# Kernel tuning notes

Measured on AMD Instinct MI355X. Metric: run time of the kernel, lower is better.

## Reference

```python
import jax, jax.numpy as jnp
import numpy as np

BASE_R = 0.1      # base_radius (compared against squared distances)
K = 20            # PositionEncoder k
H = 0.1           # dilated_ball_query bandwidth
EPS_BN = 1e-5


def _gelu(x):
    return jax.nn.gelu(x, approximate=False)  # torch nn.GELU default (erf)


def _bn(x, g, b):
    # eval-mode BatchNorm (running_mean=0, running_var=1), channel axis = 1
    shape = (1, -1) + (1,) * (x.ndim - 2)
    scale = g / np.float32(np.sqrt(1.0 + EPS_BN))
    return x * scale.reshape(shape) + b.reshape(shape)


def _conv1x1(x, w):
    # pointwise conv (no bias): w [out_c, in_c], x [B, in_c, ...]
    return jnp.einsum('oc,bc...->bo...', w, x)


def _l1norm(x, axis):
    # F.normalize(p=1): divide by L1 norm clamped to 1e-12
    return x / jnp.maximum(jnp.sum(jnp.abs(x), axis=axis, keepdims=True), 1e-12)


def _forward(xyz, w_q, g_q, b_q, w_k, g_k, b_k, w_v, g_v, b_v,
             w_pe, b_pe, g_pe, bb_pe, w_m1, g_m1, b_m1, w_m2, g_m2, b_m2,
             w_out, g_out, b_out):
    B, _, N = xyz.shape
    # ---- pairwise squared distances [B,N,N] ----
    sq = jnp.sum(xyz * xyz, axis=1)
    dist = -2.0 * jnp.einsum('bcn,bcm->bnm', xyz, xyz) + sq[:, :, None] + sq[:, None, :]
    # ---- dilated ball query (sigma=1) ----
    gauss = jnp.exp(-dist / (2.0 * H * H))
    kd = jnp.sum(gauss, axis=-1, keepdims=True)                 # [B,N,1]
    kd_score = kd / (jnp.max(kd, axis=1, keepdims=True) + 1e-9)
    radius = BASE_R + BASE_R * kd_score                         # max_radius = 2*base
    keep = dist < radius                                        # [B,N,N]
    # ---- masked attention (emb_cent == emb_x == cat(xyz, xyz)) ----
    emb = jnp.concatenate([xyz, xyz], axis=1)                   # [B,6,N]
    q = _bn(_conv1x1(emb, w_q), g_q, b_q)                       # [B,1,N]
    k_ = _bn(_conv1x1(emb, w_k), g_k, b_k)                      # [B,1,N]
    scores = jnp.einsum('bhn,bhm->bnm', q, k_)                  # [B,N,N]
    scores = jnp.where(keep, scores, -1e9)
    adj = jax.nn.softmax(scores, axis=-1)
    adj = _l1norm(_l1norm(adj, 1), -1)                          # doubly L1-normalized
    # ---- graph smoothing + value conv ----
    smoothed = jnp.einsum('bcn,bnm->bcm', xyz, adj)
    variation = smoothed - xyz
    v = _bn(_conv1x1(jnp.concatenate([variation, xyz], axis=1), w_v), g_v, b_v)  # [B,64,N]
    # ---- position encoder: ball-query top-k neighbor gather ----
    ar = jnp.arange(N, dtype=jnp.int32)[None, None, :]
    idx = jnp.where(dist > radius, N, ar)                       # mark out-of-ball with N
    idx = jnp.sort(idx, axis=-1)[:, :, :K]                      # k nearest-index in-ball
    idx = jnp.where(idx == N, idx[:, :, :1], idx)               # pad with first neighbor
    grouped = jax.vmap(lambda f, i: f[:, i])(xyz, idx)          # [B,3,N,K]
    pts = jnp.broadcast_to(xyz[:, :, :, None], grouped.shape)
    pf = jnp.concatenate([pts, grouped, grouped - pts], axis=1)  # [B,9,N,K]
    pf = _conv1x1(pf, w_pe) + b_pe[None, :, None, None]          # conv2d 1x1 with bias
    pf = _gelu(_bn(pf, g_pe, bb_pe))
    pf = jnp.max(pf, axis=-1)                                    # [B,out/8,N]
    pf = _gelu(_bn(_conv1x1(pf, w_m1), g_m1, b_m1))              # [B,out/4,N]
    pos = _bn(_conv1x1(pf, w_m2), g_m2, b_m2)                    # [B,out,N]
    out = _gelu(v + pos)
    return _bn(_conv1x1(out, w_out), g_out, b_out)               # [B,32,N]


def setup_inputs() -> dict:
    key = jax.random.key(0)
    ks = iter(jax.random.split(key, 40))
    B, N, OC = 4, 4096, 64

    def w(shape):
        return jax.random.normal(next(ks), shape, jnp.float32) / np.float32(np.sqrt(shape[-1]))

    def gb(c):
        g = 1.0 + 0.1 * jax.random.normal(next(ks), (c,), jnp.float32)
        b = 0.1 * jax.random.normal(next(ks), (c,), jnp.float32)
        return g, b

    xyz = jax.random.uniform(next(ks), (B, 3, N), jnp.float32)
    g_q, b_q = gb(1)
    g_k, b_k = gb(1)
    g_v, b_v = gb(OC)
    g_pe, bb_pe = gb(OC // 8)
    g_m1, b_m1 = gb(OC // 4)
    g_m2, b_m2 = gb(OC)
    g_out, b_out = gb(32)
    return {
        'xyz': xyz,
        'w_q': w((1, 6)), 'g_q': g_q, 'b_q': b_q,
        'w_k': w((1, 6)), 'g_k': g_k, 'b_k': b_k,
        'w_v': w((OC, 6)), 'g_v': g_v, 'b_v': b_v,
        'w_pe': w((OC // 8, 9)), 'b_pe': 0.1 * jax.random.normal(next(ks), (OC // 8,), jnp.float32),
        'g_pe': g_pe, 'bb_pe': bb_pe,
        'w_m1': w((OC // 4, OC // 8)), 'g_m1': g_m1, 'b_m1': b_m1,
        'w_m2': w((OC, OC // 4)), 'g_m2': g_m2, 'b_m2': b_m2,
        'w_out': w((32, OC)), 'g_out': g_out, 'b_out': b_out,
    }


def reference(xyz, w_q, g_q, b_q, w_k, g_k, b_k, w_v, g_v, b_v,
              w_pe, b_pe, g_pe, bb_pe, w_m1, g_m1, b_m1, w_m2, g_m2, b_m2,
              w_out, g_out, b_out):
    return _forward(xyz, w_q, g_q, b_q, w_k, g_k, b_k, w_v, g_v, b_v,
                    w_pe, b_pe, g_pe, bb_pe, w_m1, g_m1, b_m1, w_m2, g_m2, b_m2,
                    w_out, g_out, b_out)
```

## Files before the change

### kernel.cpp

```cpp
#include <hip/hip_runtime.h>
#include <math.h>

#define BB 4
#define NN 4096
#define KNBR 20
#define BN (BB * NN)
#define NSLICE 8
#define SLEN (NN / NSLICE)
#define JPW (SLEN / 16)

#define LOG2E 1.44269504088896340736f

typedef __attribute__((ext_vector_type(2))) float v2f;

__device__ __forceinline__ v2f fma2(v2f a, v2f b, v2f c) {
    return __builtin_elementwise_fma(a, b, c);
}
__device__ __forceinline__ v2f splat2(float s) { v2f r; r.x = s; r.y = s; return r; }

__device__ __forceinline__ float gelu_f(float x) {
    return 0.5f * x * (1.0f + erff(x * 0.70710678118654752440f));
}

__device__ __forceinline__ float4 mkrec(const float* __restrict__ xb, int n) {
    float x = xb[n], y = xb[NN + n], z = xb[2 * NN + n];
    float sq = fmaf(x, x, fmaf(y, y, z * z));
    return make_float4(x, y, z, sq);
}

__global__ void k0_prep(const float* __restrict__ xyz, float4* __restrict__ pts4) {
    int t = blockIdx.x * blockDim.x + threadIdx.x;
    if (t >= BN) return;
    int b = t / NN, n = t % NN;
    pts4[t] = mkrec(xyz + (size_t)b * 3 * NN, n);
}


__global__ __launch_bounds__(1024, 8)
void p1_kd(const float4* __restrict__ pts4, float* __restrict__ part) {
    __shared__ float s_red[16][256];
    int tid = threadIdx.x;
    int wave = __builtin_amdgcn_readfirstlane(tid >> 6);
    int lane = tid & 63;
    int g = blockIdx.x >> 3, slice = blockIdx.x & 7;
    int b = g >> 4;
    const float4* rb = pts4 + (size_t)b * NN + slice * SLEN + wave * JPW;
    v2f frx[2], fry[2], frz[2], frw[2];
    v2f acc[2] = {splat2(0.f), splat2(0.f)};
    #pragma unroll
    for (int h = 0; h < 2; ++h) {
        float4 r0 = pts4[g * 256 + (2 * h) * 64 + lane];
        float4 r1 = pts4[g * 256 + (2 * h + 1) * 64 + lane];
        frx[h].x = r0.x; frx[h].y = r1.x;
        fry[h].x = r0.y; fry[h].y = r1.y;
        frz[h].x = r0.z; frz[h].y = r1.z;
        frw[h].x = r0.w; frw[h].y = r1.w;
    }
    const v2f m2 = splat2(-2.0f);
    const float C1 = -50.0f * LOG2E;
    #pragma unroll 4
    for (int j = 0; j < JPW; ++j) {
        float4 fc = rb[j];
        #pragma unroll
        for (int h = 0; h < 2; ++h) {
            v2f dot = frx[h] * fc.x + fry[h] * fc.y + frz[h] * fc.z;
            v2f d = fma2(m2, dot, frw[h]) + fc.w;
            v2f arg = d * C1;
            acc[h].x += __builtin_amdgcn_exp2f(arg.x);
            acc[h].y += __builtin_amdgcn_exp2f(arg.y);
        }
    }
    #pragma unroll
    for (int h = 0; h < 2; ++h) {
        s_red[wave][(2 * h) * 64 + lane] = acc[h].x;
        s_red[wave][(2 * h + 1) * 64 + lane] = acc[h].y;
    }
    __syncthreads();
    if (tid < 256) {
        float s = 0.f;
        #pragma unroll
        for (int w = 0; w < 16; ++w) s += s_red[w][tid];
        part[slice * BN + g * 256 + tid] = s;
    }
}

__global__ void k2_radius(const float* __restrict__ part, const float4* __restrict__ pts4,
                          const float* __restrict__ w_q, const float* __restrict__ g_q, const float* __restrict__ b_q,
                          const float* __restrict__ w_k, const float* __restrict__ g_k, const float* __restrict__ b_k,
                          float4* __restrict__ recB) {
    int b = blockIdx.x;
    int t = threadIdx.x;
    const float invs = rsqrtf(1.0f + 1e-5f);
    float kdv[4];
    float mx = -1e30f;
    #pragma unroll
    for (int j = 0; j < 4; ++j) {
        int n = b * NN + j * 1024 + t;
        float s = 0.f;
        #pragma unroll
        for (int c = 0; c < NSLICE; ++c) s += part[c * BN + n];
        kdv[j] = s;
        mx = fmaxf(mx, s);
    }
    __shared__ float red[1024];
    red[t] = mx;
    __syncthreads();
    for (int s = 512; s > 0; s >>= 1) {
        if (t < s) red[t] = fmaxf(red[t], red[t + s]);
        __syncthreads();
    }
    float kmax = red[0];
    #pragma unroll
    for (int j = 0; j < 4; ++j) {
        int n = b * NN + j * 1024 + t;
        float rad = 0.1f + 0.1f * (kdv[j] / (kmax + 1e-9f));
        float4 r = pts4[n];
        float qr = r.x * (w_q[0] + w_q[3]) + r.y * (w_q[1] + w_q[4]) + r.z * (w_q[2] + w_q[5]);
        float kr = r.x * (w_k[0] + w_k[3]) + r.y * (w_k[1] + w_k[4]) + r.z * (w_k[2] + w_k[5]);
        float q = qr * (g_q[0] * invs) + b_q[0];
        float k = kr * (g_k[0] * invs) + b_k[0];
        recB[2 * n] = r;
        recB[2 * n + 1] = make_float4(k, q, rad, 0.f);
    }
}

__global__ __launch_bounds__(1024, 8)
void p3_Zk7(const float4* __restrict__ recB, float* __restrict__ part,
            int* __restrict__ idxg) {
    __shared__ float s_red[16][256];
    int tid = threadIdx.x;
    int wave = __builtin_amdgcn_readfirstlane(tid >> 6);
    int lane = tid & 63;
    int g = blockIdx.x >> 3, slice = blockIdx.x & 7;
    int b = g >> 4;
    const float4* rb = recB + ((size_t)b * NN + slice * SLEN + wave * JPW) * 2;
    v2f frx[2], fry[2], frz[2], frw[2], ql2[2], rad[2];
    v2f acc[2] = {splat2(0.f), splat2(0.f)};
    #pragma unroll
    for (int h = 0; h < 2; ++h) {
        int r0i = g * 256 + (2 * h) * 64 + lane;
        int r1i = g * 256 + (2 * h + 1) * 64 + lane;
        float4 r0 = recB[2 * r0i], a0 = recB[2 * r0i + 1];
        float4 r1 = recB[2 * r1i], a1 = recB[2 * r1i + 1];
        frx[h].x = r0.x; frx[h].y = r1.x;
        fry[h].x = r0.y; fry[h].y = r1.y;
        frz[h].x = r0.z; frz[h].y = r1.z;
        frw[h].x = r0.w; frw[h].y = r1.w;
        ql2[h].x = a0.y * LOG2E; ql2[h].y = a1.y * LOG2E;
        rad[h].x = a0.z; rad[h].y = a1.z;
    }
    const v2f m2 = splat2(-2.0f);
    #pragma unroll 4
    for (int j = 0; j < JPW; ++j) {
        float4 fc = rb[2 * j];
        float4 an = rb[2 * j + 1];
        #pragma unroll
        for (int h = 0; h < 2; ++h) {
            v2f dot = frx[h] * fc.x + fry[h] * fc.y + frz[h] * fc.z;
            v2f d = fma2(m2, dot, frw[h]) + fc.w;
            v2f arg = ql2[h] * an.x;
            float e0 = __builtin_amdgcn_exp2f(arg.x);
            float e1 = __builtin_amdgcn_exp2f(arg.y);
            acc[h].x += (d.x < rad[h].x) ? e0 : 0.f;
            acc[h].y += (d.y < rad[h].y) ? e1 : 0.f;
        }
    }
    #pragma unroll
    for (int h = 0; h < 2; ++h) {
        s_red[wave][(2 * h) * 64 + lane] = acc[h].x;
        s_red[wave][(2 * h + 1) * 64 + lane] = acc[h].y;
    }
    __syncthreads();
    if (tid < 256) {
        float s = 0.f;
        #pragma unroll
        for (int w = 0; w < 16; ++w) s += s_red[w][tid];
        part[slice * BN + g * 256 + tid] = s;
    }
    int gw = blockIdx.x * 16 + wave;
    for (int rr = 0; rr < 2; ++rr) {
        int row7 = gw * 2 + rr;
        int b7 = row7 / NN;
        const float4* p7 = recB + (size_t)b7 * NN * 2;
        float4 f7 = recB[2 * row7];
        float rad7 = recB[2 * row7 + 1].z;
        int total = 0, firstm = 0;
        bool have = false;
        unsigned long long lmask = (1ULL << lane) - 1ULL;
        for (int i = 0; i < NN / 64 && total < KNBR; ++i) {
            int m = i * 64 + lane;
            float4 fc = p7[2 * m];
            float dot = f7.x * fc.x + f7.y * fc.y + f7.z * fc.z;
            float d = fmaf(-2.0f, dot, f7.w) + fc.w;
            bool inb = !(d > rad7);
            unsigned long long mask = __ballot(inb);
            if (!have && mask != 0ULL) {
                int src7 = __ffsll(mask) - 1;
                firstm = __shfl(m, src7);
                have = true;
            }
            int pos = total + (int)__popcll(mask & lmask);
            if (inb && pos < KNBR) idxg[(size_t)row7 * KNBR + pos] = m;
            total += (int)__popcll(mask);
        }
        if (total < KNBR && lane >= total && lane < KNBR)
            idxg[(size_t)row7 * KNBR + lane] = firstm;
    }
}

__global__ __launch_bounds__(1024, 8)
void p4_colsum(const float4* __restrict__ recB, const float* __restrict__ part3,
               float* __restrict__ part) {
    __shared__ float s_red[16][256];
    __shared__ float s_lnZ[SLEN];
    int tid = threadIdx.x;
    int wave = __builtin_amdgcn_readfirstlane(tid >> 6);
    int lane = tid & 63;
    int g = blockIdx.x >> 3, slice = blockIdx.x & 7;
    int b = g >> 4;
    if (tid < SLEN) {
        int gn = b * NN + slice * SLEN + tid;
        float s = 0.f;
        #pragma unroll
        for (int c = 0; c < NSLICE; ++c) s += part3[c * BN + gn];
        s_lnZ[tid] = __log2f(s);
    }
    const float4* rb = recB + ((size_t)b * NN + slice * SLEN + wave * JPW) * 2;
    v2f fcx[2], fcy[2], fcz[2], fcw[2], km2[2];
    v2f acc[2] = {splat2(0.f), splat2(0.f)};
    #pragma unroll
    for (int h = 0; h < 2; ++h) {
        int c0 = g * 256 + (2 * h) * 64 + lane;
        int c1 = g * 256 + (2 * h + 1) * 64 + lane;
        float4 r0 = recB[2 * c0], a0 = recB[2 * c0 + 1];
        float4 r1 = recB[2 * c1], a1 = recB[2 * c1 + 1];
        fcx[h].x = r0.x; fcx[h].y = r1.x;
        fcy[h].x = r0.y; fcy[h].y = r1.y;
        fcz[h].x = r0.z; fcz[h].y = r1.z;
        fcw[h].x = r0.w; fcw[h].y = r1.w;
        km2[h].x = a0.x * LOG2E; km2[h].y = a1.x * LOG2E;
    }
    __syncthreads();
    const v2f m2 = splat2(-2.0f);
    #pragma unroll 4
    for (int j = 0; j < JPW; ++j) {
        float4 fc = rb[2 * j];
        float4 an = rb[2 * j + 1];
        float lnZ2 = s_lnZ[wave * JPW + j];
        #pragma unroll
        for (int h = 0; h < 2; ++h) {
            v2f dot = fcx[h] * fc.x + fcy[h] * fc.y + fcz[h] * fc.z;
            v2f d = fma2(m2, dot, splat2(fc.w)) + fcw[h];
            v2f arg = fma2(splat2(an.y), km2[h], splat2(-lnZ2));
            float e0 = __builtin_amdgcn_exp2f(arg.x);
            float e1 = __builtin_amdgcn_exp2f(arg.y);
            acc[h].x += (d.x < an.z) ? e0 : 0.f;
            acc[h].y += (d.y < an.z) ? e1 : 0.f;
        }
    }
    #pragma unroll
    for (int h = 0; h < 2; ++h) {
        s_red[wave][(2 * h) * 64 + lane] = acc[h].x;
        s_red[wave][(2 * h + 1) * 64 + lane] = acc[h].y;
    }
    __syncthreads();
    if (tid < 256) {
        float s = 0.f;
        #pragma unroll
        for (int w = 0; w < 16; ++w) s += s_red[w][tid];
        part[slice * BN + g * 256 + tid] = s;
    }
}

__global__ __launch_bounds__(1024, 8)
void p5_rs(const float4* __restrict__ recB, const float* __restrict__ part5,
           float* __restrict__ part) {
    __shared__ float s_red[16][256];
    __shared__ float s_lnc[SLEN];
    int tid = threadIdx.x;
    int wave = __builtin_amdgcn_readfirstlane(tid >> 6);
    int lane = tid & 63;
    int g = blockIdx.x >> 3, slice = blockIdx.x & 7;
    int b = g >> 4;
    if (tid < SLEN) {
        int gm = b * NN + slice * SLEN + tid;
        float s = 0.f;
        #pragma unroll
        for (int c = 0; c < NSLICE; ++c) s += part5[c * BN + gm];
        s_lnc[tid] = __log2f(fmaxf(s, 1e-12f));
    }
    const float4* rb = recB + ((size_t)b * NN + slice * SLEN + wave * JPW) * 2;
    v2f frx[2], fry[2], frz[2], frw[2], ql2[2], rad[2];
    v2f acc[2] = {splat2(0.f), splat2(0.f)};
    #pragma unroll
    for (int h = 0; h < 2; ++h) {
        int r0i = g * 256 + (2 * h) * 64 + lane;
        int r1i = g * 256 + (2 * h + 1) * 64 + lane;
        float4 r0 = recB[2 * r0i], a0 = recB[2 * r0i + 1];
        float4 r1 = recB[2 * r1i], a1 = recB[2 * r1i + 1];
        frx[h].x = r0.x; frx[h].y = r1.x;
        fry[h].x = r0.y; fry[h].y = r1.y;
        frz[h].x = r0.z; frz[h].y = r1.z;
        frw[h].x = r0.w; frw[h].y = r1.w;
        ql2[h].x = a0.y * LOG2E; ql2[h].y = a1.y * LOG2E;
        rad[h].x = a0.z; rad[h].y = a1.z;
    }
    __syncthreads();
    const v2f m2 = splat2(-2.0f);
    #pragma unroll 4
    for (int j = 0; j < JPW; ++j) {
        float4 fc = rb[2 * j];
        float km = rb[2 * j + 1].x;
        float lnc2 = s_lnc[wave * JPW + j];
        #pragma unroll
        for (int h = 0; h < 2; ++h) {
            v2f dot = frx[h] * fc.x + fry[h] * fc.y + frz[h] * fc.z;
            v2f d = fma2(m2, dot, frw[h]) + fc.w;
            v2f arg = fma2(splat2(km), ql2[h], splat2(-lnc2));
            float e0 = __builtin_amdgcn_exp2f(arg.x);
            float e1 = __builtin_amdgcn_exp2f(arg.y);
            acc[h].x += (d.x < rad[h].x) ? e0 : 0.f;
            acc[h].y += (d.y < rad[h].y) ? e1 : 0.f;
        }
    }
    #pragma unroll
    for (int h = 0; h < 2; ++h) {
        s_red[wave][(2 * h) * 64 + lane] = acc[h].x;
        s_red[wave][(2 * h + 1) * 64 + lane] = acc[h].y;
    }
    __syncthreads();
    if (tid < 256) {
        float s = 0.f;
        #pragma unroll
        for (int w = 0; w < 16; ++w) s += s_red[w][tid];
        part[slice * BN + g * 256 + tid] = s;
    }
}

__global__ __launch_bounds__(1024, 8)
void p6_smooth(const float4* __restrict__ recB, const float* __restrict__ part3,
               const float* __restrict__ part7,
               float* __restrict__ partx, float* __restrict__ party,
               float* __restrict__ partz) {
    __shared__ float s_rx[16][256];
    __shared__ float s_ry[16][256];
    __shared__ float s_rz[16][256];
    __shared__ float s_w[SLEN];
    int tid = threadIdx.x;
    int wave = __builtin_amdgcn_readfirstlane(tid >> 6);
    int lane = tid & 63;
    int g = blockIdx.x >> 3, slice = blockIdx.x & 7;
    int b = g >> 4;
    if (tid < SLEN) {
        int gn = b * NN + slice * SLEN + tid;
        float sZ = 0.f, s7 = 0.f;
        #pragma unroll
        for (int c = 0; c < NSLICE; ++c) {
            sZ += part3[c * BN + gn];
            s7 += part7[c * BN + gn];
        }
        float rs = fmaxf(s7 / sZ, 1e-12f);
        s_w[tid] = __log2f(sZ) + __log2f(rs);
    }
    const float4* rb = recB + ((size_t)b * NN + slice * SLEN + wave * JPW) * 2;
    v2f fcx[2], fcy[2], fcz[2], fcw[2], km2[2];
    v2f ax[2] = {splat2(0.f), splat2(0.f)};
    v2f ay[2] = {splat2(0.f), splat2(0.f)};
    v2f az[2] = {splat2(0.f), splat2(0.f)};
    #pragma unroll
    for (int h = 0; h < 2; ++h) {
        int c0 = g * 256 + (2 * h) * 64 + lane;
        int c1 = g * 256 + (2 * h + 1) * 64 + lane;
        float4 r0 = recB[2 * c0], a0 = recB[2 * c0 + 1];
        float4 r1 = recB[2 * c1], a1 = recB[2 * c1 + 1];
        fcx[h].x = r0.x; fcx[h].y = r1.x;
        fcy[h].x = r0.y; fcy[h].y = r1.y;
        fcz[h].x = r0.z; fcz[h].y = r1.z;
        fcw[h].x = r0.w; fcw[h].y = r1.w;
        km2[h].x = a0.x * LOG2E; km2[h].y = a1.x * LOG2E;
    }
    __syncthreads();
    const v2f m2 = splat2(-2.0f);
    #pragma unroll 2
    for (int j = 0; j < JPW; ++j) {
        float4 fc = rb[2 * j];
        float4 an = rb[2 * j + 1];
        float w2j = s_w[wave * JPW + j];
        #pragma unroll
        for (int h = 0; h < 2; ++h) {
            v2f dot = fcx[h] * fc.x + fcy[h] * fc.y + fcz[h] * fc.z;
            v2f d = fma2(m2, dot, splat2(fc.w)) + fcw[h];
            v2f arg = fma2(splat2(an.y), km2[h], splat2(-w2j));
            float e0 = __builtin_amdgcn_exp2f(arg.x);
            float e1 = __builtin_amdgcn_exp2f(arg.y);
            v2f w;
            w.x = (d.x < an.z) ? e0 : 0.f;
            w.y = (d.y < an.z) ? e1 : 0.f;
            ax[h] = fma2(splat2(fc.x), w, ax[h]);
            ay[h] = fma2(splat2(fc.y), w, ay[h]);
            az[h] = fma2(splat2(fc.z), w, az[h]);
        }
    }
    #pragma unroll
    for (int h = 0; h < 2; ++h) {
        s_rx[wave][(2 * h) * 64 + lane] = ax[h].x;
        s_rx[wave][(2 * h + 1) * 64 + lane] = ax[h].y;
        s_ry[wave][(2 * h) * 64 + lane] = ay[h].x;
        s_ry[wave][(2 * h + 1) * 64 + lane] = ay[h].y;
        s_rz[wave][(2 * h) * 64 + lane] = az[h].x;
        s_rz[wave][(2 * h + 1) * 64 + lane] = az[h].y;
    }
    __syncthreads();
    if (tid < 256) {
        float sx = 0.f, sy = 0.f, sz = 0.f;
        #pragma unroll
        for (int w = 0; w < 16; ++w) {
            sx += s_rx[w][tid];
            sy += s_ry[w][tid];
            sz += s_rz[w][tid];
        }
        int o = slice * BN + g * 256 + tid;
        partx[o] = sx;
        party[o] = sy;
        partz[o] = sz;
    }
}

__global__ void k8_final(const float* __restrict__ xyz,
                         const float* __restrict__ partx, const float* __restrict__ party,
                         const float* __restrict__ partz, const float* __restrict__ part5,
                         const int* __restrict__ idxg,
                         const float* __restrict__ w_v, const float* __restrict__ g_v, const float* __restrict__ b_v,
                         const float* __restrict__ w_pe, const float* __restrict__ b_pe,
                         const float* __restrict__ g_pe, const float* __restrict__ bb_pe,
                         const float* __restrict__ w_m1, const float* __restrict__ g_m1, const float* __restrict__ b_m1,
                         const float* __restrict__ w_m2, const float* __restrict__ g_m2, const float* __restrict__ b_m2,
                         const float* __restrict__ w_out, const float* __restrict__ g_out, const float* __restrict__ b_out,
                         float* __restrict__ out) {
    __shared__ float s_pf8[32][9];
    __shared__ float s_pf16[32][17];
    __shared__ float s_g64[32][65];
    int tid = threadIdx.x;
    int ptL = tid >> 3, o = tid & 7;
    int p = blockIdx.x * 32 + ptL;
    int b = p / NN, n = p % NN;
    const float* xb = xyz + (size_t)b * 3 * NN;
    float x = xb[n], y = xb[NN + n], z = xb[2 * NN + n];
    const float invs = rsqrtf(1.0f + 1e-5f);

    float w0 = w_pe[o * 9 + 0], w1 = w_pe[o * 9 + 1], w2 = w_pe[o * 9 + 2];
    float w3 = w_pe[o * 9 + 3], w4 = w_pe[o * 9 + 4], w5 = w_pe[o * 9 + 5];
    float w6 = w_pe[o * 9 + 6], w7 = w_pe[o * 9 + 7], w8 = w_pe[o * 9 + 8];
    float bp = b_pe[o], gp = g_pe[o] * invs, bbp = bb_pe[o];
    float mx = -1e30f;
    for (int kk = 0; kk < KNBR; ++kk) {
        int j = idxg[(size_t)p * KNBR + kk];
        float gx = xb[j], gy = xb[NN + j], gz = xb[2 * NN + j];
        float dx = gx - x, dy = gy - y, dz = gz - z;
        float s = w0 * x + w1 * y + w2 * z + w3 * gx + w4 * gy + w5 * gz
                + w6 * dx + w7 * dy + w8 * dz + bp;
        s = gelu_f(s * gp + bbp);
        mx = fmaxf(mx, s);
    }
    s_pf8[ptL][o] = mx;
    __syncthreads();

    #pragma unroll
    for (int rr = 0; rr < 2; ++rr) {
        int r = o + rr * 8;
        const float* w = w_m1 + r * 8;
        float s = 0.f;
        #pragma unroll
        for (int c = 0; c < 8; ++c) s += w[c] * s_pf8[ptL][c];
        s_pf16[ptL][r] = gelu_f(s * (g_m1[r] * invs) + b_m1[r]);
    }
    __syncthreads();

    float cs = 0.f, sx = 0.f, sy = 0.f, sz = 0.f;
    #pragma unroll
    for (int c = 0; c < NSLICE; ++c) {
        cs += part5[c * BN + p];
        sx += partx[c * BN + p];
        sy += party[c * BN + p];
        sz += partz[c * BN + p];
    }
    float inv = 1.0f / fmaxf(cs, 1e-12f);
    float vx = sx * inv - x, vy = sy * inv - y, vz = sz * inv - z;
    #pragma unroll
    for (int i = 0; i < 8; ++i) {
        int ch = o * 8 + i;
        const float* wm = w_m2 + ch * 16;
        float pos = 0.f;
        #pragma unroll
        for (int c = 0; c < 16; ++c) pos += wm[c] * s_pf16[ptL][c];
        pos = pos * (g_m2[ch] * invs) + b_m2[ch];
        const float* wv = w_v + ch * 6;
        float vv = wv[0] * vx + wv[1] * vy + wv[2] * vz + wv[3] * x + wv[4] * y + wv[5] * z;
        vv = vv * (g_v[ch] * invs) + b_v[ch];
        s_g64[ptL][ch] = gelu_f(vv + pos);
    }
    __syncthreads();

    #pragma unroll
    for (int i = 0; i < 4; ++i) {
        int ch = o * 4 + i;
        const float* w = w_out + ch * 64;
        float s = 0.f;
        #pragma unroll
        for (int c = 0; c < 64; ++c) s += w[c] * s_g64[ptL][c];
        out[((size_t)b * 32 + ch) * NN + n] = s * (g_out[ch] * invs) + b_out[ch];
    }
}

extern "C" void kernel_launch(void* const* d_in, const int* in_sizes, int n_in,
                              void* d_out, int out_size, void* d_ws, size_t ws_size,
                              hipStream_t stream) {
    const float* xyz  = (const float*)d_in[0];
    const float* w_q  = (const float*)d_in[1];
    const float* g_q  = (const float*)d_in[2];
    const float* b_q  = (const float*)d_in[3];
    const float* w_k  = (const float*)d_in[4];
    const float* g_k  = (const float*)d_in[5];
    const float* b_k  = (const float*)d_in[6];
    const float* w_v  = (const float*)d_in[7];
    const float* g_v  = (const float*)d_in[8];
    const float* b_v  = (const float*)d_in[9];
    const float* w_pe = (const float*)d_in[10];
    const float* b_pe = (const float*)d_in[11];
    const float* g_pe = (const float*)d_in[12];
    const float* bb_pe= (const float*)d_in[13];
    const float* w_m1 = (const float*)d_in[14];
    const float* g_m1 = (const float*)d_in[15];
    const float* b_m1 = (const float*)d_in[16];
    const float* w_m2 = (const float*)d_in[17];
    const float* g_m2 = (const float*)d_in[18];
    const float* b_m2 = (const float*)d_in[19];
    const float* w_out= (const float*)d_in[20];
    const float* g_out= (const float*)d_in[21];
    const float* b_out= (const float*)d_in[22];

    float* ws = (float*)d_ws;
    float4* pts4   = (float4*)ws;
    float4* recB   = (float4*)(ws + (size_t)4  * BN);
    int*    idxg   = (int*)   (ws + (size_t)12 * BN);
    float*  part1  = ws + (size_t)32 * BN;
    float*  part3  = ws + (size_t)40 * BN;
    float*  part5  = ws + (size_t)48 * BN;
    float*  part7  = ws + (size_t)56 * BN;
    float*  partx  = ws + (size_t)64 * BN;
    float*  party  = ws + (size_t)72 * BN;
    float*  partz  = ws + (size_t)80 * BN;

    const int PB = (BN / 256) * NSLICE;

    k0_prep<<<BN / 256, 256, 0, stream>>>(xyz, pts4);
    p1_kd<<<PB, 1024, 0, stream>>>(pts4, part1);
    k2_radius<<<BB, 1024, 0, stream>>>(part1, pts4, w_q, g_q, b_q, w_k, g_k, b_k, recB);
    p3_Zk7<<<PB, 1024, 0, stream>>>(recB, part3, idxg);
    p4_colsum<<<PB, 1024, 0, stream>>>(recB, part3, part5);
    p5_rs<<<PB, 1024, 0, stream>>>(recB, part5, part7);
    p6_smooth<<<PB, 1024, 0, stream>>>(recB, part3, part7, partx, party, partz);
    k8_final<<<BN / 32, 256, 0, stream>>>(xyz, partx, party, partz, part5, idxg,
                                          w_v, g_v, b_v,
                                          w_pe, b_pe, g_pe, bb_pe,
                                          w_m1, g_m1, b_m1,
                                          w_m2, g_m2, b_m2,
                                          w_out, g_out, b_out,
                                          (float*)d_out);
}
```

Baseline: 234.9 us.

## Retile pairwise passes to 512-thread blocks with 8 rows per lane and 32 slices

```diff
diff --git a/kernel.cpp b/kernel.cpp
--- a/kernel.cpp
+++ b/kernel.cpp
@@ -5,9 +5,9 @@
 #define NN 4096
 #define KNBR 20
 #define BN (BB * NN)
-#define NSLICE 8
+#define NSLICE 32
 #define SLEN (NN / NSLICE)
-#define JPW (SLEN / 16)
+#define JPW (SLEN / 8)
 
 #define LOG2E 1.44269504088896340736f
 
@@ -36,21 +36,21 @@
 }
 
 
-__global__ __launch_bounds__(1024, 8)
+__global__ __launch_bounds__(512, 6)
 void p1_kd(const float4* __restrict__ pts4, float* __restrict__ part) {
-    __shared__ float s_red[16][256];
+    __shared__ float s_red[8][512];
     int tid = threadIdx.x;
     int wave = __builtin_amdgcn_readfirstlane(tid >> 6);
     int lane = tid & 63;
-    int g = blockIdx.x >> 3, slice = blockIdx.x & 7;
-    int b = g >> 4;
+    int g = blockIdx.x >> 5, slice = blockIdx.x & 31;
+    int b = g >> 3;
     const float4* rb = pts4 + (size_t)b * NN + slice * SLEN + wave * JPW;
-    v2f frx[2], fry[2], frz[2], frw[2];
-    v2f acc[2] = {splat2(0.f), splat2(0.f)};
-    #pragma unroll
-    for (int h = 0; h < 2; ++h) {
-        float4 r0 = pts4[g * 256 + (2 * h) * 64 + lane];
-        float4 r1 = pts4[g * 256 + (2 * h + 1) * 64 + lane];
+    v2f frx[4], fry[4], frz[4], frw[4];
+    v2f acc[4] = {splat2(0.f), splat2(0.f), splat2(0.f), splat2(0.f)};
+    #pragma unroll
+    for (int h = 0; h < 4; ++h) {
+        float4 r0 = pts4[g * 512 + (2 * h) * 64 + lane];
+        float4 r1 = pts4[g * 512 + (2 * h + 1) * 64 + lane];
         frx[h].x = r0.x; frx[h].y = r1.x;
         fry[h].x = r0.y; fry[h].y = r1.y;
         frz[h].x = r0.z; frz[h].y = r1.z;
@@ -58,11 +58,11 @@
     }
     const v2f m2 = splat2(-2.0f);
     const float C1 = -50.0f * LOG2E;
-    #pragma unroll 4
+    #pragma unroll 2
     for (int j = 0; j < JPW; ++j) {
         float4 fc = rb[j];
         #pragma unroll
-        for (int h = 0; h < 2; ++h) {
+        for (int h = 0; h < 4; ++h) {
             v2f dot = frx[h] * fc.x + fry[h] * fc.y + frz[h] * fc.z;
             v2f d = fma2(m2, dot, frw[h]) + fc.w;
             v2f arg = d * C1;
@@ -71,16 +71,16 @@
         }
     }
     #pragma unroll
-    for (int h = 0; h < 2; ++h) {
+    for (int h = 0; h < 4; ++h) {
         s_red[wave][(2 * h) * 64 + lane] = acc[h].x;
         s_red[wave][(2 * h + 1) * 64 + lane] = acc[h].y;
     }
     __syncthreads();
-    if (tid < 256) {
-        float s = 0.f;
-        #pragma unroll
-        for (int w = 0; w < 16; ++w) s += s_red[w][tid];
-        part[slice * BN + g * 256 + tid] = s;
+    {
+        float s = 0.f;
+        #pragma unroll
+        for (int w = 0; w < 8; ++w) s += s_red[w][tid];
+        part[slice * BN + g * 512 + tid] = s;
     }
 }
 
@@ -124,22 +124,22 @@
     }
 }
 
-__global__ __launch_bounds__(1024, 8)
+__global__ __launch_bounds__(512, 6)
 void p3_Zk7(const float4* __restrict__ recB, float* __restrict__ part,
             int* __restrict__ idxg) {
-    __shared__ float s_red[16][256];
+    __shared__ float s_red[8][512];
     int tid = threadIdx.x;
     int wave = __builtin_amdgcn_readfirstlane(tid >> 6);
     int lane = tid & 63;
-    int g = blockIdx.x >> 3, slice = blockIdx.x & 7;
-    int b = g >> 4;
+    int g = blockIdx.x >> 5, slice = blockIdx.x & 31;
+    int b = g >> 3;
     const float4* rb = recB + ((size_t)b * NN + slice * SLEN + wave * JPW) * 2;
-    v2f frx[2], fry[2], frz[2], frw[2], ql2[2], rad[2];
-    v2f acc[2] = {splat2(0.f), splat2(0.f)};
-    #pragma unroll
-    for (int h = 0; h < 2; ++h) {
-        int r0i = g * 256 + (2 * h) * 64 + lane;
-        int r1i = g * 256 + (2 * h + 1) * 64 + lane;
+    v2f frx[4], fry[4], frz[4], frw[4], ql2[4], rad[4];
+    v2f acc[4] = {splat2(0.f), splat2(0.f), splat2(0.f), splat2(0.f)};
+    #pragma unroll
+    for (int h = 0; h < 4; ++h) {
+        int r0i = g * 512 + (2 * h) * 64 + lane;
+        int r1i = g * 512 + (2 * h + 1) * 64 + lane;
         float4 r0 = recB[2 * r0i], a0 = recB[2 * r0i + 1];
         float4 r1 = recB[2 * r1i], a1 = recB[2 * r1i + 1];
         frx[h].x = r0.x; frx[h].y = r1.x;
@@ -150,12 +150,12 @@
         rad[h].x = a0.z; rad[h].y = a1.z;
     }
     const v2f m2 = splat2(-2.0f);
-    #pragma unroll 4
+    #pragma unroll 2
     for (int j = 0; j < JPW; ++j) {
         float4 fc = rb[2 * j];
         float4 an = rb[2 * j + 1];
         #pragma unroll
-        for (int h = 0; h < 2; ++h) {
+        for (int h = 0; h < 4; ++h) {
             v2f dot = frx[h] * fc.x + fry[h] * fc.y + frz[h] * fc.z;
             v2f d = fma2(m2, dot, frw[h]) + fc.w;
             v2f arg = ql2[h] * an.x;
@@ -166,18 +166,18 @@
         }
     }
     #pragma unroll
-    for (int h = 0; h < 2; ++h) {
+    for (int h = 0; h < 4; ++h) {
         s_red[wave][(2 * h) * 64 + lane] = acc[h].x;
         s_red[wave][(2 * h + 1) * 64 + lane] = acc[h].y;
     }
     __syncthreads();
-    if (tid < 256) {
-        float s = 0.f;
-        #pragma unroll
-        for (int w = 0; w < 16; ++w) s += s_red[w][tid];
-        part[slice * BN + g * 256 + tid] = s;
-    }
-    int gw = blockIdx.x * 16 + wave;
+    {
+        float s = 0.f;
+        #pragma unroll
+        for (int w = 0; w < 8; ++w) s += s_red[w][tid];
+        part[slice * BN + g * 512 + tid] = s;
+    }
+    int gw = blockIdx.x * 8 + wave;
     for (int rr = 0; rr < 2; ++rr) {
         int row7 = gw * 2 + rr;
         int b7 = row7 / NN;
@@ -208,16 +208,16 @@
     }
 }
 
-__global__ __launch_bounds__(1024, 8)
+__global__ __launch_bounds__(512, 6)
 void p4_colsum(const float4* __restrict__ recB, const float* __restrict__ part3,
                float* __restrict__ part) {
-    __shared__ float s_red[16][256];
+    __shared__ float s_red[8][512];
     __shared__ float s_lnZ[SLEN];
     int tid = threadIdx.x;
     int wave = __builtin_amdgcn_readfirstlane(tid >> 6);
     int lane = tid & 63;
-    int g = blockIdx.x >> 3, slice = blockIdx.x & 7;
-    int b = g >> 4;
+    int g = blockIdx.x >> 5, slice = blockIdx.x & 31;
+    int b = g >> 3;
     if (tid < SLEN) {
         int gn = b * NN + slice * SLEN + tid;
         float s = 0.f;
@@ -226,12 +226,12 @@
         s_lnZ[tid] = __log2f(s);
     }
     const float4* rb = recB + ((size_t)b * NN + slice * SLEN + wave * JPW) * 2;
-    v2f fcx[2], fcy[2], fcz[2], fcw[2], km2[2];
-    v2f acc[2] = {splat2(0.f), splat2(0.f)};
-    #pragma unroll
-    for (int h = 0; h < 2; ++h) {
-        int c0 = g * 256 + (2 * h) * 64 + lane;
-        int c1 = g * 256 + (2 * h + 1) * 64 + lane;
+    v2f fcx[4], fcy[4], fcz[4], fcw[4], km2[4];
+    v2f acc[4] = {splat2(0.f), splat2(0.f), splat2(0.f), splat2(0.f)};
+    #pragma unroll
+    for (int h = 0; h < 4; ++h) {
+        int c0 = g * 512 + (2 * h) * 64 + lane;
+        int c1 = g * 512 + (2 * h + 1) * 64 + lane;
         float4 r0 = recB[2 * c0], a0 = recB[2 * c0 + 1];
         float4 r1 = recB[2 * c1], a1 = recB[2 * c1 + 1];
         fcx[h].x = r0.x; fcx[h].y = r1.x;
@@ -242,13 +242,13 @@
     }
     __syncthreads();
     const v2f m2 = splat2(-2.0f);
-    #pragma unroll 4
+    #pragma unroll 2
     for (int j = 0; j < JPW; ++j) {
         float4 fc = rb[2 * j];
         float4 an = rb[2 * j + 1];
         float lnZ2 = s_lnZ[wave * JPW + j];
         #pragma unroll
-        for (int h = 0; h < 2; ++h) {
+        for (int h = 0; h < 4; ++h) {
             v2f dot = fcx[h] * fc.x + fcy[h] * fc.y + fcz[h] * fc.z;
             v2f d = fma2(m2, dot, splat2(fc.w)) + fcw[h];
             v2f arg = fma2(splat2(an.y), km2[h], splat2(-lnZ2));
@@ -259,29 +259,29 @@
         }
     }
     #pragma unroll
-    for (int h = 0; h < 2; ++h) {
+    for (int h = 0; h < 4; ++h) {
         s_red[wave][(2 * h) * 64 + lane] = acc[h].x;
         s_red[wave][(2 * h + 1) * 64 + lane] = acc[h].y;
     }
     __syncthreads();
-    if (tid < 256) {
-        float s = 0.f;
-        #pragma unroll
-        for (int w = 0; w < 16; ++w) s += s_red[w][tid];
-        part[slice * BN + g * 256 + tid] = s;
-    }
-}
-
-__global__ __launch_bounds__(1024, 8)
+    {
+        float s = 0.f;
+        #pragma unroll
+        for (int w = 0; w < 8; ++w) s += s_red[w][tid];
+        part[slice * BN + g * 512 + tid] = s;
+    }
+}
+
+__global__ __launch_bounds__(512, 6)
 void p5_rs(const float4* __restrict__ recB, const float* __restrict__ part5,
            float* __restrict__ part) {
-    __shared__ float s_red[16][256];
+    __shared__ float s_red[8][512];
     __shared__ float s_lnc[SLEN];
     int tid = threadIdx.x;
     int wave = __builtin_amdgcn_readfirstlane(tid >> 6);
     int lane = tid & 63;
-    int g = blockIdx.x >> 3, slice = blockIdx.x & 7;
-    int b = g >> 4;
+    int g = blockIdx.x >> 5, slice = blockIdx.x & 31;
+    int b = g >> 3;
     if (tid < SLEN) {
         int gm = b * NN + slice * SLEN + tid;
         float s = 0.f;
@@ -290,12 +290,12 @@
         s_lnc[tid] = __log2f(fmaxf(s, 1e-12f));
     }
     const float4* rb = recB + ((size_t)b * NN + slice * SLEN + wave * JPW) * 2;
-    v2f frx[2], fry[2], frz[2], frw[2], ql2[2], rad[2];
-    v2f acc[2] = {splat2(0.f), splat2(0.f)};
-    #pragma unroll
-    for (int h = 0; h < 2; ++h) {
-        int r0i = g * 256 + (2 * h) * 64 + lane;
-        int r1i = g * 256 + (2 * h + 1) * 64 + lane;
+    v2f frx[4], fry[4], frz[4], frw[4], ql2[4], rad[4];
+    v2f acc[4] = {splat2(0.f), splat2(0.f), splat2(0.f), splat2(0.f)};
+    #pragma unroll
+    for (int h = 0; h < 4; ++h) {
+        int r0i = g * 512 + (2 * h) * 64 + lane;
+        int r1i = g * 512 + (2 * h + 1) * 64 + lane;
         float4 r0 = recB[2 * r0i], a0 = recB[2 * r0i + 1];
         float4 r1 = recB[2 * r1i], a1 = recB[2 * r1i + 1];
         frx[h].x = r0.x; frx[h].y = r1.x;
@@ -307,13 +307,13 @@
     }
     __syncthreads();
     const v2f m2 = splat2(-2.0f);
-    #pragma unroll 4
+    #pragma unroll 2
     for (int j = 0; j < JPW; ++j) {
         float4 fc = rb[2 * j];
         float km = rb[2 * j + 1].x;
         float lnc2 = s_lnc[wave * JPW + j];
         #pragma unroll
-        for (int h = 0; h < 2; ++h) {
+        for (int h = 0; h < 4; ++h) {
             v2f dot = frx[h] * fc.x + fry[h] * fc.y + frz[h] * fc.z;
             v2f d = fma2(m2, dot, frw[h]) + fc.w;
             v2f arg = fma2(splat2(km), ql2[h], splat2(-lnc2));
@@ -324,32 +324,32 @@
         }
     }
     #pragma unroll
-    for (int h = 0; h < 2; ++h) {
+    for (int h = 0; h < 4; ++h) {
         s_red[wave][(2 * h) * 64 + lane] = acc[h].x;
         s_red[wave][(2 * h + 1) * 64 + lane] = acc[h].y;
     }
     __syncthreads();
-    if (tid < 256) {
-        float s = 0.f;
-        #pragma unroll
-        for (int w = 0; w < 16; ++w) s += s_red[w][tid];
-        part[slice * BN + g * 256 + tid] = s;
-    }
-}
-
-__global__ __launch_bounds__(1024, 8)
+    {
+        float s = 0.f;
+        #pragma unroll
+        for (int w = 0; w < 8; ++w) s += s_red[w][tid];
+        part[slice * BN + g * 512 + tid] = s;
+    }
+}
+
+__global__ __launch_bounds__(512, 6)
 void p6_smooth(const float4* __restrict__ recB, const float* __restrict__ part3,
                const float* __restrict__ part7,
                float* __restrict__ partx, float* __restrict__ party,
                float* __restrict__ partz) {
-    __shared__ float s_rx[16][256];
-    __shared__ float s_ry[16][256];
-    __shared__ float s_rz[16][256];
+    __shared__ float s_rx[8][256];
+    __shared__ float s_ry[8][256];
+    __shared__ float s_rz[8][256];
     __shared__ float s_w[SLEN];
     int tid = threadIdx.x;
     int wave = __builtin_amdgcn_readfirstlane(tid >> 6);
     int lane = tid & 63;
-    int g = blockIdx.x >> 3, slice = blockIdx.x & 7;
+    int g = blockIdx.x >> 5, slice = blockIdx.x & 31;
     int b = g >> 4;
     if (tid < SLEN) {
         int gn = b * NN + slice * SLEN + tid;
@@ -414,7 +414,7 @@
     if (tid < 256) {
         float sx = 0.f, sy = 0.f, sz = 0.f;
         #pragma unroll
-        for (int w = 0; w < 16; ++w) {
+        for (int w = 0; w < 8; ++w) {
             sx += s_rx[w][tid];
             sy += s_ry[w][tid];
             sz += s_rz[w][tid];
@@ -440,6 +440,7 @@
     __shared__ float s_pf8[32][9];
     __shared__ float s_pf16[32][17];
     __shared__ float s_g64[32][65];
+    __shared__ float s_acc[32][8][4];
     int tid = threadIdx.x;
     int ptL = tid >> 3, o = tid & 7;
     int p = blockIdx.x * 32 + ptL;
@@ -447,6 +448,21 @@
     const float* xb = xyz + (size_t)b * 3 * NN;
     float x = xb[n], y = xb[NN + n], z = xb[2 * NN + n];
     const float invs = rsqrtf(1.0f + 1e-5f);
+
+    {
+        float cs = 0.f, sx = 0.f, sy = 0.f, sz = 0.f;
+        #pragma unroll
+        for (int c = o; c < NSLICE; c += 8) {
+            cs += part5[c * BN + p];
+            sx += partx[c * BN + p];
+            sy += party[c * BN + p];
+            sz += partz[c * BN + p];
+        }
+        s_acc[ptL][o][0] = cs;
+        s_acc[ptL][o][1] = sx;
+        s_acc[ptL][o][2] = sy;
+        s_acc[ptL][o][3] = sz;
+    }
 
     float w0 = w_pe[o * 9 + 0], w1 = w_pe[o * 9 + 1], w2 = w_pe[o * 9 + 2];
     float w3 = w_pe[o * 9 + 3], w4 = w_pe[o * 9 + 4], w5 = w_pe[o * 9 + 5];
@@ -478,11 +494,11 @@
 
     float cs = 0.f, sx = 0.f, sy = 0.f, sz = 0.f;
     #pragma unroll
-    for (int c = 0; c < NSLICE; ++c) {
-        cs += part5[c * BN + p];
-        sx += partx[c * BN + p];
-        sy += party[c * BN + p];
-        sz += partz[c * BN + p];
+    for (int w = 0; w < 8; ++w) {
+        cs += s_acc[ptL][w][0];
+        sx += s_acc[ptL][w][1];
+        sy += s_acc[ptL][w][2];
+        sz += s_acc[ptL][w][3];
     }
     float inv = 1.0f / fmaxf(cs, 1e-12f);
     float vx = sx * inv - x, vy = sy * inv - y, vz = sz * inv - z;
@@ -543,23 +559,24 @@
     float4* pts4   = (float4*)ws;
     float4* recB   = (float4*)(ws + (size_t)4  * BN);
     int*    idxg   = (int*)   (ws + (size_t)12 * BN);
-    float*  part1  = ws + (size_t)32 * BN;
-    float*  part3  = ws + (size_t)40 * BN;
-    float*  part5  = ws + (size_t)48 * BN;
-    float*  part7  = ws + (size_t)56 * BN;
-    float*  partx  = ws + (size_t)64 * BN;
-    float*  party  = ws + (size_t)72 * BN;
-    float*  partz  = ws + (size_t)80 * BN;
-
-    const int PB = (BN / 256) * NSLICE;
+    float*  part1  = ws + (size_t)32  * BN;
+    float*  part3  = ws + (size_t)64  * BN;
+    float*  part5  = ws + (size_t)96  * BN;
+    float*  part7  = ws + (size_t)128 * BN;
+    float*  partx  = ws + (size_t)160 * BN;
+    float*  party  = ws + (size_t)192 * BN;
+    float*  partz  = ws + (size_t)224 * BN;
+
+    const int PA = (BN / 512) * NSLICE;
+    const int PBC = (BN / 256) * NSLICE;
 
     k0_prep<<<BN / 256, 256, 0, stream>>>(xyz, pts4);
-    p1_kd<<<PB, 1024, 0, stream>>>(pts4, part1);
+    p1_kd<<<PA, 512, 0, stream>>>(pts4, part1);
     k2_radius<<<BB, 1024, 0, stream>>>(part1, pts4, w_q, g_q, b_q, w_k, g_k, b_k, recB);
-    p3_Zk7<<<PB, 1024, 0, stream>>>(recB, part3, idxg);
-    p4_colsum<<<PB, 1024, 0, stream>>>(recB, part3, part5);
-    p5_rs<<<PB, 1024, 0, stream>>>(recB, part5, part7);
-    p6_smooth<<<PB, 1024, 0, stream>>>(recB, part3, part7, partx, party, partz);
+    p3_Zk7<<<PA, 512, 0, stream>>>(recB, part3, idxg);
+    p4_colsum<<<PA, 512, 0, stream>>>(recB, part3, part5);
+    p5_rs<<<PA, 512, 0, stream>>>(recB, part5, part7);
+    p6_smooth<<<PBC, 512, 0, stream>>>(recB, part3, part7, partx, party, partz);
     k8_final<<<BN / 32, 256, 0, stream>>>(xyz, partx, party, partz, part5, idxg,
                                           w_v, g_v, b_v,
                                           w_pe, b_pe, g_pe, bb_pe,
```

Measured after the change: 249.1 us. +6.0%, slower.
